# Kernel optimization log

Hardware: AMD Instinct MI355X
Metric: run time of the kernel (lower is better)

Reference implementation:

```python
import math
import jax, jax.numpy as jnp
import numpy as np

V, BS, L, C, H, B, T = 50257, 2048, 4, 768, 12, 2, 2048
D = C // H


def layer_norm(x, g, b, eps=1e-5):
    m = x.mean(-1, keepdims=True)
    v = ((x - m) ** 2).mean(-1, keepdims=True)
    return (x - m) / jnp.sqrt(v + eps) * g + b


def setup_inputs() -> dict:
    key = jax.random.key(0)
    ks = jax.random.split(key, 10)
    s = 0.02
    inp = {}
    inp["idx"] = jax.random.randint(ks[0], (B, T), 0, V)
    inp["tok_emb"] = jax.random.normal(ks[1], (V, C), jnp.float32) * s
    inp["pos_emb"] = jax.random.normal(ks[2], (BS, C), jnp.float32) * s
    inp["ln1_g"] = jnp.ones((L, C)); inp["ln1_b"] = jnp.zeros((L, C))
    inp["qkv_w"] = jax.random.normal(ks[3], (L, C, 3 * C), jnp.float32) * s
    inp["qkv_b"] = jnp.zeros((L, 3 * C))
    inp["aproj_w"] = jax.random.normal(ks[4], (L, C, C), jnp.float32) * s
    inp["aproj_b"] = jnp.zeros((L, C))
    inp["ln2_g"] = jnp.ones((L, C)); inp["ln2_b"] = jnp.zeros((L, C))
    inp["fc_w"] = jax.random.normal(ks[5], (L, C, 4 * C), jnp.float32) * s
    inp["fc_b"] = jnp.zeros((L, 4 * C))
    inp["mproj_w"] = jax.random.normal(ks[6], (L, 4 * C, C), jnp.float32) * s
    inp["mproj_b"] = jnp.zeros((L, C))
    inp["lnf_g"] = jnp.ones((C,)); inp["lnf_b"] = jnp.zeros((C,))
    inp["head_w"] = jax.random.normal(ks[7], (C, V), jnp.float32) * s
    return inp


def reference(idx, tok_emb, pos_emb, ln1_g, ln1_b, qkv_w, qkv_b, aproj_w, aproj_b,
              ln2_g, ln2_b, fc_w, fc_b, mproj_w, mproj_b, lnf_g, lnf_b, head_w):
    b, t = idx.shape
    x = tok_emb[idx] + pos_emb[:t][None]  # [B,T,C]; dropout p=0 -> identity
    mask = jnp.tril(jnp.ones((t, t), bool))  # causal
    neg_inf = jnp.finfo(x.dtype).min
    n_layer = qkv_w.shape[0]
    for l in range(n_layer):
        h = layer_norm(x, ln1_g[l], ln1_b[l])
        qkv = h @ qkv_w[l] + qkv_b[l]  # [B,T,3C]
        q, k, v = jnp.split(qkv, 3, axis=-1)
        q = q.reshape(b, t, H, D).transpose(0, 2, 1, 3)  # [B,H,T,D]
        k = k.reshape(b, t, H, D).transpose(0, 2, 1, 3)
        v = v.reshape(b, t, H, D).transpose(0, 2, 1, 3)
        att = jnp.einsum('bhqd,bhkd->bhqk', q, k) / math.sqrt(D)
        att = jnp.where(mask, att, neg_inf)
        att = jax.nn.softmax(att, axis=-1)
        y = jnp.einsum('bhqk,bhkd->bhqd', att, v)
        y = y.transpose(0, 2, 1, 3).reshape(b, t, C)
        x = x + (y @ aproj_w[l] + aproj_b[l])
        h2 = layer_norm(x, ln2_g[l], ln2_b[l])
        hid = jax.nn.gelu(h2 @ fc_w[l] + fc_b[l], approximate=False)  # exact erf GELU (torch default)
        x = x + (hid @ mproj_w[l] + mproj_b[l])
    x = layer_norm(x, lnf_g, lnf_b)
    logits = x @ head_w  # [B,T,V]
    return logits
```

## Files before the change

kernel.cpp:

```cpp
#include <hip/hip_runtime.h>
#include <cstdint>
#include <cstddef>

#define Tn 2048
#define Bn 2
#define Hn 12
#define Cn 768
#define Ln 4
#define Vn 50257

typedef unsigned short ushort_t;
typedef __attribute__((ext_vector_type(8))) __bf16 bf16x8;
typedef __attribute__((ext_vector_type(8))) unsigned short u16x8;
typedef __attribute__((ext_vector_type(4))) unsigned short u16x4;
typedef __attribute__((ext_vector_type(4))) float f32x4;

static constexpr size_t QKV_ELEMS = (size_t)Bn * Hn * Tn * 64;
static constexpr size_t OFF_QKV = 0;
static constexpr size_t OFF_APROJ = 1769472;
static constexpr size_t OFF_FC = 2359296;
static constexpr size_t OFF_MPROJ = 4718592;

__device__ inline unsigned short f2bf(float f) {
  unsigned int u = __float_as_uint(f);
  unsigned int r = (u + 0x7fffu + ((u >> 16) & 1u)) >> 16;
  return (unsigned short)r;
}

__device__ inline f32x4 zero4() { f32x4 z; z[0]=0.f; z[1]=0.f; z[2]=0.f; z[3]=0.f; return z; }

__device__ inline void gload_lds16(const ushort_t* g, ushort_t* l) {
  __builtin_amdgcn_global_load_lds(
      (const __attribute__((address_space(1))) void*)g,
      (__attribute__((address_space(3))) void*)l, 16, 0, 0);
}

__device__ inline int swz_lin() {
  int nbm = gridDim.x;
  int lin = blockIdx.y * nbm + blockIdx.x;
  int nwg = nbm * gridDim.y;
  int q = nwg >> 3, r = nwg & 7, x = lin & 7, p = lin >> 3;
  return (x < r ? x * (q + 1) : r * (q + 1) + (x - r) * q) + p;
}

__global__ __launch_bounds__(192) void embed_kernel(const int* __restrict__ idx,
    const float* __restrict__ tok, const float* __restrict__ pos, float* __restrict__ x) {
  int row = blockIdx.x;
  int t = row & (Tn - 1);
  int token = idx[row];
  const f32x4* tr = (const f32x4*)(tok + (size_t)token * Cn);
  const f32x4* pr = (const f32x4*)(pos + (size_t)t * Cn);
  f32x4* xr = (f32x4*)(x + (size_t)row * Cn);
  xr[threadIdx.x] = tr[threadIdx.x] + pr[threadIdx.x];
}

__global__ __launch_bounds__(256) void ln_kernel(const float* __restrict__ x,
    const float* __restrict__ gam, const float* __restrict__ bet, ushort_t* __restrict__ out) {
  const int wv = threadIdx.x >> 6, lane = threadIdx.x & 63;
  const int row = blockIdx.x * 4 + wv;
  const f32x4* xr = (const f32x4*)(x + (size_t)row * Cn);
  f32x4 v[3]; float s = 0.f, s2 = 0.f;
  #pragma unroll
  for (int e = 0; e < 3; ++e) {
    v[e] = xr[lane + e*64];
    #pragma unroll
    for (int j = 0; j < 4; ++j) { s += v[e][j]; s2 += v[e][j]*v[e][j]; }
  }
  #pragma unroll
  for (int off = 32; off >= 1; off >>= 1) { s += __shfl_xor(s, off); s2 += __shfl_xor(s2, off); }
  float mean = s * (1.f / Cn);
  float var  = s2 * (1.f / Cn) - mean * mean;
  float rstd = rsqrtf(var + 1e-5f);
  const f32x4* g4 = (const f32x4*)gam;
  const f32x4* b4 = (const f32x4*)bet;
  u16x4* o4 = (u16x4*)(out + (size_t)row * Cn);
  #pragma unroll
  for (int e = 0; e < 3; ++e) {
    f32x4 gv = g4[lane + e*64], bv = b4[lane + e*64];
    u16x4 o;
    #pragma unroll
    for (int j = 0; j < 4; ++j) o[j] = f2bf((v[e][j] - mean) * rstd * gv[j] + bv[j]);
    o4[lane + e*64] = o;
  }
}

__global__ __launch_bounds__(256) void tcvt_kernel(const float* __restrict__ in,
    ushort_t* __restrict__ out, int K, int N, int Npad) {
  __shared__ float tile[32][33];
  int n0 = blockIdx.x * 32, k0 = blockIdx.y * 32;
  int tx = threadIdx.x, ty = threadIdx.y;
  #pragma unroll
  for (int r = 0; r < 4; ++r) {
    int k = k0 + ty + 8*r;
    int n = n0 + tx;
    tile[ty + 8*r][tx] = (n < N) ? in[(size_t)k * N + n] : 0.f;
  }
  __syncthreads();
  #pragma unroll
  for (int r = 0; r < 4; ++r) {
    int n = n0 + ty + 8*r;
    out[(size_t)n * K + k0 + tx] = f2bf(tile[tx][ty + 8*r]);
  }
}

__global__ __launch_bounds__(256) void tcvt4_kernel(const float* __restrict__ qkvp,
    const float* __restrict__ aprojp, const float* __restrict__ fcp,
    const float* __restrict__ mprojp, ushort_t* __restrict__ wT) {
  __shared__ float tile[32][33];
  int bid = blockIdx.x;
  const float* in; int K, N, tilesX, local; size_t ooff;
  if (bid < 1728)      { in = qkvp;   K = 768;  N = 2304; tilesX = 72; ooff = OFF_QKV;   local = bid; }
  else if (bid < 2304) { in = aprojp; K = 768;  N = 768;  tilesX = 24; ooff = OFF_APROJ; local = bid - 1728; }
  else if (bid < 4608) { in = fcp;    K = 768;  N = 3072; tilesX = 96; ooff = OFF_FC;    local = bid - 2304; }
  else                 { in = mprojp; K = 3072; N = 768;  tilesX = 24; ooff = OFF_MPROJ; local = bid - 4608; }
  int n0 = (local % tilesX) * 32, k0 = (local / tilesX) * 32;
  int tx = threadIdx.x, ty = threadIdx.y;
  ushort_t* out = wT + ooff;
  #pragma unroll
  for (int r = 0; r < 4; ++r)
    tile[ty + 8*r][tx] = in[(size_t)(k0 + ty + 8*r) * N + n0 + tx];
  __syncthreads();
  #pragma unroll
  for (int r = 0; r < 4; ++r)
    out[(size_t)(n0 + ty + 8*r) * K + k0 + tx] = f2bf(tile[tx][ty + 8*r]);
}

__global__ __launch_bounds__(256) void vtrans_kernel(const ushort_t* __restrict__ vin,
                                                     ushort_t* __restrict__ vout) {
  __shared__ ushort_t tile[64][65];
  int t0 = blockIdx.x * 64;
  size_t bh = blockIdx.y;
  const ushort_t* src = vin + (bh * Tn + t0) * 64;
  int row = threadIdx.x >> 2, c0 = (threadIdx.x & 3) * 16;
  u16x8 a = *(const u16x8*)&src[(size_t)row * 64 + c0];
  u16x8 b = *(const u16x8*)&src[(size_t)row * 64 + c0 + 8];
  #pragma unroll
  for (int j = 0; j < 8; ++j) { tile[row][c0 + j] = a[j]; tile[row][c0 + 8 + j] = b[j]; }
  __syncthreads();
  int d = threadIdx.x >> 2, tq = (threadIdx.x & 3) * 16;
  u16x8 o0, o1;
  #pragma unroll
  for (int j = 0; j < 8; ++j) { o0[j] = tile[tq + j][d]; o1[j] = tile[tq + 8 + j][d]; }
  ushort_t* dst = vout + (bh * 64 + d) * Tn + t0 + tq;
  *(u16x8*)&dst[0] = o0;
  *(u16x8*)&dst[8] = o1;
}

__global__ __launch_bounds__(512, 2) void gemm256_kernel(
    const ushort_t* __restrict__ A, const ushort_t* __restrict__ Bt,
    const float* __restrict__ bias, float* __restrict__ outp,
    int M, int N, int K) {
  __shared__ ushort_t lds[3 * 16384];
  const int t = threadIdx.x;
  const int w = t >> 6, l = t & 63, lo = l & 15, g = l >> 4;
  const int wm = w >> 2, wn = w & 3;

  int bm, bn;
  {
    int seq = swz_lin();
    int gsz = 8 * gridDim.y;
    int grp = seq / gsz;
    int t2 = seq - grp * gsz;
    bn = t2 >> 3;
    bm = grp * 8 + (t2 & 7);
  }

  const ushort_t* gAb = A  + (size_t)bm * 256 * K;
  const ushort_t* gBb = Bt + (size_t)bn * 256 * K;

  f32x4 acc[8][4];
  #pragma unroll
  for (int i = 0; i < 8; ++i)
    #pragma unroll
    for (int j = 0; j < 4; ++j) acc[i][j] = zero4();

  auto stage = [&](int kt, int buf) {
    const int k0 = kt << 5;
    #pragma unroll
    for (int j = 0; j < 2; ++j) {
      const int q = j * 512 + t;
      const int r = q >> 2;
      const int cc = ((q & 3) ^ ((r >> 1) & 3)) << 3;
      gload_lds16(gAb + (size_t)r * K + k0 + cc,
                  &lds[buf * 16384 + j * 4096 + w * 512]);
      gload_lds16(gBb + (size_t)r * K + k0 + cc,
                  &lds[buf * 16384 + 8192 + j * 4096 + w * 512]);
    }
  };
  const int csw = ((lo >> 1) & 3) << 3;
  auto compute = [&](int buf) {
    const ushort_t* as = &lds[buf * 16384];
    const ushort_t* bs = &lds[buf * 16384 + 8192];
    bf16x8 af[8], bfr[4];
    #pragma unroll
    for (int mi = 0; mi < 8; ++mi)
      af[mi] = *(const bf16x8*)&as[(wm*128 + mi*16 + lo) * 32 + ((g*8) ^ csw)];
    #pragma unroll
    for (int ni = 0; ni < 4; ++ni)
      bfr[ni] = *(const bf16x8*)&bs[(wn*64 + ni*16 + lo) * 32 + ((g*8) ^ csw)];
    __builtin_amdgcn_s_setprio(1);
    #pragma unroll
    for (int mi = 0; mi < 8; ++mi)
      #pragma unroll
      for (int ni = 0; ni < 4; ++ni)
        acc[mi][ni] = __builtin_amdgcn_mfma_f32_16x16x32_bf16(af[mi], bfr[ni], acc[mi][ni], 0, 0, 0);
    __builtin_amdgcn_s_setprio(0);
  };

  const int NK = K >> 5;
  stage(0, 0); stage(1, 1); stage(2, 2);
  asm volatile("s_waitcnt vmcnt(8)" ::: "memory");
  __builtin_amdgcn_s_barrier();

  int buf = 0;
  #pragma unroll 1
  for (int kt = 0; kt < NK; ++kt) {
    compute(buf);
    asm volatile("s_waitcnt lgkmcnt(0)" ::: "memory");
    __builtin_amdgcn_s_barrier();
    if (kt + 3 < NK) {
      stage(kt + 3, buf);
      asm volatile("s_waitcnt vmcnt(8)" ::: "memory");
    } else if (kt + 2 < NK) {
      asm volatile("s_waitcnt vmcnt(4)" ::: "memory");
    } else {
      asm volatile("s_waitcnt vmcnt(0)" ::: "memory");
    }
    __builtin_amdgcn_s_barrier();
    buf = (buf == 2) ? 0 : buf + 1;
  }

  #pragma unroll
  for (int mi = 0; mi < 8; ++mi) {
    #pragma unroll
    for (int ni = 0; ni < 4; ++ni) {
      int colg = bn*256 + wn*64 + ni*16 + lo;
      if (colg < N) {
        float bv = bias ? bias[colg] : 0.f;
        #pragma unroll
        for (int i = 0; i < 4; ++i) {
          int rowg = bm*256 + wm*128 + mi*16 + 4*g + i;
          outp[(size_t)rowg * N + colg] = acc[mi][ni][i] + bv;
        }
      }
    }
  }
}

template<int MODE, int TM>
__global__ __launch_bounds__(256) void gemm_kernel(
    const ushort_t* __restrict__ A, const ushort_t* __restrict__ Bt,
    const float* __restrict__ bias, void* __restrict__ outp,
    const float* __restrict__ res, int M, int N, int K) {
  constexpr int MI = TM / 32;
  constexpr int ASZ = TM * 32;
  constexpr int BUFE = ASZ + 4096;
  constexpr int LPT = TM/64 + 2;
  __shared__ ushort_t lds[3 * BUFE];
  const int t = threadIdx.x;
  int bm, bn;
  {
    int seq = swz_lin();
    const int G = 8;
    int gsz = G * gridDim.y;
    int grp = seq / gsz;
    int t2 = seq - grp * gsz;
    bn = t2 / G;
    bm = grp * G + (t2 - bn * G);
  }
  const int w = t >> 6, l = t & 63, lo = l & 15, g = l >> 4;
  const int wm = w >> 1, wn = w & 1;

  f32x4 acc[MI][4];
  #pragma unroll
  for (int i = 0; i < MI; ++i)
    #pragma unroll
    for (int j = 0; j < 4; ++j) acc[i][j] = zero4();

  const ushort_t* gAb = A  + (size_t)bm * TM * K;
  const ushort_t* gBb = Bt + (size_t)bn * 128 * K;

  auto stage = [&](int kt, int buf) {
    const int k0 = kt << 5;
    #pragma unroll
    for (int j = 0; j < TM/64; ++j) {
      const int q = j * 256 + t;
      const int r = q >> 2;
      const int cc = ((q & 3) ^ ((r >> 1) & 3)) << 3;
      gload_lds16(gAb + (size_t)r * K + k0 + cc, &lds[buf*BUFE + (j*256 + w*64)*8]);
    }
    #pragma unroll
    for (int j = 0; j < 2; ++j) {
      const int q = j * 256 + t;
      const int r = q >> 2;
      const int cc = ((q & 3) ^ ((r >> 1) & 3)) << 3;
      gload_lds16(gBb + (size_t)r * K + k0 + cc, &lds[buf*BUFE + ASZ + (j*256 + w*64)*8]);
    }
  };
  const int csw = ((lo >> 1) & 3) << 3;
  auto compute = [&](int buf) {
    const ushort_t* as = &lds[buf * BUFE];
    const ushort_t* bs = &lds[buf * BUFE + ASZ];
    bf16x8 af[MI], bfr[4];
    #pragma unroll
    for (int mi = 0; mi < MI; ++mi)
      af[mi] = *(const bf16x8*)&as[(wm*(TM/2) + mi*16 + lo) * 32 + ((g*8) ^ csw)];
    #pragma unroll
    for (int ni = 0; ni < 4; ++ni)
      bfr[ni] = *(const bf16x8*)&bs[(wn*64 + ni*16 + lo) * 32 + ((g*8) ^ csw)];
    __builtin_amdgcn_s_setprio(1);
    #pragma unroll
    for (int mi = 0; mi < MI; ++mi)
      #pragma unroll
      for (int ni = 0; ni < 4; ++ni)
        acc[mi][ni] = __builtin_amdgcn_mfma_f32_16x16x32_bf16(af[mi], bfr[ni], acc[mi][ni], 0, 0, 0);
    __builtin_amdgcn_s_setprio(0);
  };

  const int NK = K >> 5;
  stage(0, 0); stage(1, 1); stage(2, 2);
  if constexpr (LPT == 4) asm volatile("s_waitcnt vmcnt(8)" ::: "memory");
  else                    asm volatile("s_waitcnt vmcnt(6)" ::: "memory");
  __builtin_amdgcn_s_barrier();

  int buf = 0;
  #pragma unroll 1
  for (int kt = 0; kt < NK; ++kt) {
    compute(buf);
    asm volatile("s_waitcnt lgkmcnt(0)" ::: "memory");
    __builtin_amdgcn_s_barrier();
    if (kt + 3 < NK) {
      stage(kt + 3, buf);
      if constexpr (LPT == 4) asm volatile("s_waitcnt vmcnt(8)" ::: "memory");
      else                    asm volatile("s_waitcnt vmcnt(6)" ::: "memory");
    } else if (kt + 2 < NK) {
      if constexpr (LPT == 4) asm volatile("s_waitcnt vmcnt(4)" ::: "memory");
      else                    asm volatile("s_waitcnt vmcnt(3)" ::: "memory");
    } else {
      asm volatile("s_waitcnt vmcnt(0)" ::: "memory");
    }
    __builtin_amdgcn_s_barrier();
    buf = (buf == 2) ? 0 : buf + 1;
  }

  #pragma unroll
  for (int mi = 0; mi < MI; ++mi) {
    #pragma unroll
    for (int ni = 0; ni < 4; ++ni) {
      int colg = bn*128 + wn*64 + ni*16 + lo;
      if (colg < N) {
        float bv = bias ? bias[colg] : 0.f;
        #pragma unroll
        for (int i = 0; i < 4; ++i) {
          int rowg = bm*TM + wm*(TM/2) + mi*16 + 4*g + i;
          float vv = acc[mi][ni][i] + bv;
          if (MODE == 1) {
            size_t off = (size_t)rowg * N + colg;
            ((float*)outp)[off] = res[off] + vv;
          } else if (MODE == 2) {
            float ge = 0.5f * vv * (1.f + erff(vv * 0.70710678118f));
            ((ushort_t*)outp)[(size_t)rowg * N + colg] = f2bf(ge);
          } else {
            int which = colg / Cn;
            int rem = colg - which * Cn;
            int h = rem >> 6, d = rem & 63;
            int b = rowg >> 11, tt = rowg & (Tn - 1);
            ushort_t* qb = (ushort_t*)outp;
            size_t bh = (size_t)(b * Hn + h);
            size_t off = (bh * Tn + tt) * 64 + d;
            if (which == 0)      qb[off] = f2bf(vv * 0.125f);
            else if (which == 1) qb[QKV_ELEMS + off] = f2bf(vv);
            else                 qb[3*QKV_ELEMS + off] = f2bf(vv);
          }
        }
      }
    }
  }
}

__global__ __launch_bounds__(64) void attn_kernel(const ushort_t* __restrict__ qkvh,
                                                  ushort_t* __restrict__ y) {
  const int l = threadIdx.x;
  const int lo = l & 15, g = l >> 4;
  int nl = swz_lin();
  const int qt = nl & 127;
  const int bh = nl >> 7;
  const int b = bh / Hn, h = bh % Hn;
  const int q0 = qt * 16;
  const ushort_t* Qp = qkvh + (size_t)bh * Tn * 64;
  const ushort_t* Kp = qkvh + QKV_ELEMS + (size_t)bh * Tn * 64;
  const ushort_t* Vt = qkvh + 2*QKV_ELEMS + (size_t)bh * 64 * Tn;

  bf16x8 qf[2];
  #pragma unroll
  for (int ch = 0; ch < 2; ++ch)
    qf[ch] = *(const bf16x8*)&Qp[(size_t)(q0 + lo) * 64 + ch*32 + g*8];

  f32x4 of[4];
  #pragma unroll
  for (int ch = 0; ch < 4; ++ch) of[ch] = zero4();
  float m = -1e30f, lsum = 0.f;
  const int nkv = q0 + 16;
  const bool ghi = (g >= 2);
  const int lg2 = (g & 1) * 32;

  for (int kv0 = 0; kv0 < nkv; kv0 += 32) {
    bf16x8 vf[4];
    #pragma unroll
    for (int ch = 0; ch < 4; ++ch)
      vf[ch] = *(const bf16x8*)&Vt[(size_t)(ch*16 + lo) * Tn + kv0 + g*8];

    float s8[8];
    #pragma unroll
    for (int sub = 0; sub < 2; ++sub) {
      int kvb = kv0 + 16*sub;
      bf16x8 kf[2];
      #pragma unroll
      for (int ch = 0; ch < 2; ++ch)
        kf[ch] = *(const bf16x8*)&Kp[(size_t)(kvb + lo) * 64 + ch*32 + g*8];
      f32x4 st = zero4();
      st = __builtin_amdgcn_mfma_f32_16x16x32_bf16(kf[0], qf[0], st, 0, 0, 0);
      st = __builtin_amdgcn_mfma_f32_16x16x32_bf16(kf[1], qf[1], st, 0, 0, 0);
      #pragma unroll
      for (int i = 0; i < 4; ++i) {
        int kvi = kvb + 4*g + i;
        s8[sub*4 + i] = (kvi <= q0 + lo) ? st[i] : -1e30f;
      }
    }
    float tmax = s8[0];
    #pragma unroll
    for (int j = 1; j < 8; ++j) tmax = fmaxf(tmax, s8[j]);
    tmax = fmaxf(tmax, __shfl_xor(tmax, 16));
    tmax = fmaxf(tmax, __shfl_xor(tmax, 32));
    if (!__all(tmax <= m)) {
      float newm = fmaxf(m, tmax);
      float resc = __expf(m - newm);
      lsum *= resc;
      m = newm;
      #pragma unroll
      for (int i = 0; i < 4; ++i) {
        float rs = __shfl(resc, 4*g + i);
        of[0][i] *= rs; of[1][i] *= rs; of[2][i] *= rs; of[3][i] *= rs;
      }
    }
    float p8[8]; float psum = 0.f;
    #pragma unroll
    for (int j = 0; j < 8; ++j) { p8[j] = __expf(s8[j] - m); psum += p8[j]; }
    psum += __shfl_xor(psum, 16);
    psum += __shfl_xor(psum, 32);
    lsum += psum;
    unsigned int q4[4];
    #pragma unroll
    for (int c = 0; c < 4; ++c)
      asm("v_cvt_pk_bf16_f32 %0, %1, %2" : "=v"(q4[c]) : "v"(p8[2*c]), "v"(p8[2*c+1]));
    union { unsigned int wv[4]; bf16x8 v; } pu;
    #pragma unroll
    for (int j = 0; j < 4; ++j) {
      int srcLane = lo + lg2 + ((j >> 1) << 4);
      unsigned int lo_w = (unsigned int)__shfl((int)q4[j & 1], srcLane);
      unsigned int hi_w = (unsigned int)__shfl((int)q4[2 + (j & 1)], srcLane);
      pu.wv[j] = ghi ? hi_w : lo_w;
    }
    #pragma unroll
    for (int ch = 0; ch < 4; ++ch)
      of[ch] = __builtin_amdgcn_mfma_f32_16x16x32_bf16(pu.v, vf[ch], of[ch], 0, 0, 0);
  }

  #pragma unroll
  for (int i = 0; i < 4; ++i) {
    float li = 1.f / __shfl(lsum, 4*g + i);
    of[0][i] *= li; of[1][i] *= li; of[2][i] *= li; of[3][i] *= li;
  }
  ushort_t* yb = y + ((size_t)b*Tn + q0) * Cn + h*64;
  #pragma unroll
  for (int ch = 0; ch < 4; ++ch)
    #pragma unroll
    for (int i = 0; i < 4; ++i)
      yb[(size_t)(4*g + i) * Cn + ch*16 + lo] = f2bf(of[ch][i]);
}

extern "C" void kernel_launch(void* const* d_in, const int* in_sizes, int n_in,
                              void* d_out, int out_size, void* d_ws, size_t ws_size,
                              hipStream_t stream) {
  const int*   idx     = (const int*)d_in[0];
  const float* tok_emb = (const float*)d_in[1];
  const float* pos_emb = (const float*)d_in[2];
  const float* ln1_g   = (const float*)d_in[3];
  const float* ln1_b   = (const float*)d_in[4];
  const float* qkv_w   = (const float*)d_in[5];
  const float* qkv_b   = (const float*)d_in[6];
  const float* aproj_w = (const float*)d_in[7];
  const float* aproj_b = (const float*)d_in[8];
  const float* ln2_g   = (const float*)d_in[9];
  const float* ln2_b   = (const float*)d_in[10];
  const float* fc_w    = (const float*)d_in[11];
  const float* fc_b    = (const float*)d_in[12];
  const float* mproj_w = (const float*)d_in[13];
  const float* mproj_b = (const float*)d_in[14];
  const float* lnf_g   = (const float*)d_in[15];
  const float* lnf_b   = (const float*)d_in[16];
  const float* head_w  = (const float*)d_in[17];
  float* out = (float*)d_out;

  char* ws = (char*)d_ws;
  float*    x    = (float*)(ws);
  ushort_t* hA   = (ushort_t*)(ws + 12582912);
  ushort_t* hB   = (ushort_t*)(ws + 18874368);
  ushort_t* qkvh = (ushort_t*)(ws + 44040192);
  ushort_t* wT   = (ushort_t*)(ws + 69206016);

  const int M = Bn * Tn;
  dim3 tb(32, 8);

  embed_kernel<<<M, 192, 0, stream>>>(idx, tok_emb, pos_emb, x);
  for (int l = 0; l < Ln; ++l) {
    ln_kernel<<<M/4, 256, 0, stream>>>(x, ln1_g + l*Cn, ln1_b + l*Cn, hA);
    tcvt4_kernel<<<6912, tb, 0, stream>>>(qkv_w + (size_t)l*Cn*3*Cn, aproj_w + (size_t)l*Cn*Cn,
                                          fc_w + (size_t)l*Cn*4*Cn, mproj_w + (size_t)l*4*Cn*Cn, wT);
    gemm_kernel<3,128><<<dim3(M/128, 2304/128), 256, 0, stream>>>(hA, wT + OFF_QKV, qkv_b + (size_t)l*3*Cn, qkvh, nullptr, M, 2304, 768);
    vtrans_kernel<<<dim3(Tn/64, Bn*Hn), 256, 0, stream>>>(qkvh + 3*QKV_ELEMS, qkvh + 2*QKV_ELEMS);
    attn_kernel<<<dim3(128, Bn*Hn), 64, 0, stream>>>(qkvh, hA);
    gemm_kernel<1,64><<<dim3(M/64, 768/128), 256, 0, stream>>>(hA, wT + OFF_APROJ, aproj_b + (size_t)l*Cn, x, x, M, 768, 768);
    ln_kernel<<<M/4, 256, 0, stream>>>(x, ln2_g + l*Cn, ln2_b + l*Cn, hA);
    gemm_kernel<2,128><<<dim3(M/128, 3072/128), 256, 0, stream>>>(hA, wT + OFF_FC, fc_b + (size_t)l*4*Cn, hB, nullptr, M, 3072, 768);
    gemm_kernel<1,64><<<dim3(M/64, 768/128), 256, 0, stream>>>(hB, wT + OFF_MPROJ, mproj_b + (size_t)l*Cn, x, x, M, 768, 3072);
  }
  ln_kernel<<<M/4, 256, 0, stream>>>(x, lnf_g, lnf_b, hA);
  tcvt_kernel<<<dim3(50432/32, 768/32), tb, 0, stream>>>(head_w, wT, 768, Vn, 50432);
  gemm256_kernel<<<dim3(M/256, 50432/256), 512, 0, stream>>>(hA, wT, nullptr, out, M, Vn, 768);
}
```

Before: 1.691 ms.

## Process two query tiles per attention wave and batch all-layer weight conversion

The attention kernel now handles 32 query rows per wave as two 16-row tiles. Each K and V fragment load is shared by both tiles, which halves K/V traffic per query and doubles the MFMA work issued per load. Query tiles are scheduled in reverse order so the longest causal blocks start first. Separately, the four per-layer weight transpose/convert launches become a single launch before the layer loop, and a plain-store GEMM epilogue mode is added but not used. The costs are higher register pressure in the attention kernel and half as many attention blocks to fill the GPU.

```diff
diff --git a/kernel.cpp b/kernel.cpp
--- a/kernel.cpp
+++ b/kernel.cpp
@@ -20,6 +20,7 @@
 static constexpr size_t OFF_APROJ = 1769472;
 static constexpr size_t OFF_FC = 2359296;
 static constexpr size_t OFF_MPROJ = 4718592;
+static constexpr size_t PACK_SZ = 7077888;
 
 __device__ inline unsigned short f2bf(float f) {
   unsigned int u = __float_as_uint(f);
@@ -103,19 +104,21 @@
   }
 }
 
-__global__ __launch_bounds__(256) void tcvt4_kernel(const float* __restrict__ qkvp,
-    const float* __restrict__ aprojp, const float* __restrict__ fcp,
-    const float* __restrict__ mprojp, ushort_t* __restrict__ wT) {
+__global__ __launch_bounds__(256) void tcvtAll_kernel(const float* __restrict__ qkvw,
+    const float* __restrict__ aprojw, const float* __restrict__ fcw,
+    const float* __restrict__ mprojw, ushort_t* __restrict__ wT) {
   __shared__ float tile[32][33];
   int bid = blockIdx.x;
-  const float* in; int K, N, tilesX, local; size_t ooff;
-  if (bid < 1728)      { in = qkvp;   K = 768;  N = 2304; tilesX = 72; ooff = OFF_QKV;   local = bid; }
-  else if (bid < 2304) { in = aprojp; K = 768;  N = 768;  tilesX = 24; ooff = OFF_APROJ; local = bid - 1728; }
-  else if (bid < 4608) { in = fcp;    K = 768;  N = 3072; tilesX = 96; ooff = OFF_FC;    local = bid - 2304; }
-  else                 { in = mprojp; K = 3072; N = 768;  tilesX = 24; ooff = OFF_MPROJ; local = bid - 4608; }
+  const int layer = bid / 6912;
+  int local = bid - layer * 6912;
+  const float* in; int K, N, tilesX; size_t ooff;
+  if (local < 1728)      { in = qkvw   + (size_t)layer*1769472; K = 768;  N = 2304; tilesX = 72; ooff = OFF_QKV; }
+  else if (local < 2304) { in = aprojw + (size_t)layer*589824;  K = 768;  N = 768;  tilesX = 24; ooff = OFF_APROJ; local -= 1728; }
+  else if (local < 4608) { in = fcw    + (size_t)layer*2359296; K = 768;  N = 3072; tilesX = 96; ooff = OFF_FC;    local -= 2304; }
+  else                   { in = mprojw + (size_t)layer*2359296; K = 3072; N = 768;  tilesX = 24; ooff = OFF_MPROJ; local -= 4608; }
   int n0 = (local % tilesX) * 32, k0 = (local / tilesX) * 32;
   int tx = threadIdx.x, ty = threadIdx.y;
-  ushort_t* out = wT + ooff;
+  ushort_t* out = wT + (size_t)layer * PACK_SZ + ooff;
   #pragma unroll
   for (int r = 0; r < 4; ++r)
     tile[ty + 8*r][tx] = in[(size_t)(k0 + ty + 8*r) * N + n0 + tx];
@@ -354,7 +357,9 @@
         for (int i = 0; i < 4; ++i) {
           int rowg = bm*TM + wm*(TM/2) + mi*16 + 4*g + i;
           float vv = acc[mi][ni][i] + bv;
-          if (MODE == 1) {
+          if (MODE == 0) {
+            ((float*)outp)[(size_t)rowg * N + colg] = vv;
+          } else if (MODE == 1) {
             size_t off = (size_t)rowg * N + colg;
             ((float*)outp)[off] = res[off] + vv;
           } else if (MODE == 2) {
@@ -383,24 +388,26 @@
   const int l = threadIdx.x;
   const int lo = l & 15, g = l >> 4;
   int nl = swz_lin();
-  const int qt = nl & 127;
-  const int bh = nl >> 7;
+  const int qt = 63 - (nl & 63);
+  const int bh = nl >> 6;
   const int b = bh / Hn, h = bh % Hn;
-  const int q0 = qt * 16;
+  const int q0 = qt * 32;
   const ushort_t* Qp = qkvh + (size_t)bh * Tn * 64;
   const ushort_t* Kp = qkvh + QKV_ELEMS + (size_t)bh * Tn * 64;
   const ushort_t* Vt = qkvh + 2*QKV_ELEMS + (size_t)bh * 64 * Tn;
 
-  bf16x8 qf[2];
-  #pragma unroll
-  for (int ch = 0; ch < 2; ++ch)
-    qf[ch] = *(const bf16x8*)&Qp[(size_t)(q0 + lo) * 64 + ch*32 + g*8];
-
-  f32x4 of[4];
-  #pragma unroll
-  for (int ch = 0; ch < 4; ++ch) of[ch] = zero4();
-  float m = -1e30f, lsum = 0.f;
-  const int nkv = q0 + 16;
+  bf16x8 qf0[2], qf1[2];
+  #pragma unroll
+  for (int ch = 0; ch < 2; ++ch) {
+    qf0[ch] = *(const bf16x8*)&Qp[(size_t)(q0 + lo) * 64 + ch*32 + g*8];
+    qf1[ch] = *(const bf16x8*)&Qp[(size_t)(q0 + 16 + lo) * 64 + ch*32 + g*8];
+  }
+
+  f32x4 of0[4], of1[4];
+  #pragma unroll
+  for (int ch = 0; ch < 4; ++ch) { of0[ch] = zero4(); of1[ch] = zero4(); }
+  float m0 = -1e30f, m1 = -1e30f, ls0 = 0.f, ls1 = 0.f;
+  const int nkv = q0 + 32;
   const bool ghi = (g >= 2);
   const int lg2 = (g & 1) * 32;
 
@@ -410,7 +417,7 @@
     for (int ch = 0; ch < 4; ++ch)
       vf[ch] = *(const bf16x8*)&Vt[(size_t)(ch*16 + lo) * Tn + kv0 + g*8];
 
-    float s8[8];
+    float s80[8], s81[8];
     #pragma unroll
     for (int sub = 0; sub < 2; ++sub) {
       int kvb = kv0 + 16*sub;
@@ -418,65 +425,99 @@
       #pragma unroll
       for (int ch = 0; ch < 2; ++ch)
         kf[ch] = *(const bf16x8*)&Kp[(size_t)(kvb + lo) * 64 + ch*32 + g*8];
-      f32x4 st = zero4();
-      st = __builtin_amdgcn_mfma_f32_16x16x32_bf16(kf[0], qf[0], st, 0, 0, 0);
-      st = __builtin_amdgcn_mfma_f32_16x16x32_bf16(kf[1], qf[1], st, 0, 0, 0);
+      f32x4 st0 = zero4(), st1 = zero4();
+      st0 = __builtin_amdgcn_mfma_f32_16x16x32_bf16(kf[0], qf0[0], st0, 0, 0, 0);
+      st0 = __builtin_amdgcn_mfma_f32_16x16x32_bf16(kf[1], qf0[1], st0, 0, 0, 0);
+      st1 = __builtin_amdgcn_mfma_f32_16x16x32_bf16(kf[0], qf1[0], st1, 0, 0, 0);
+      st1 = __builtin_amdgcn_mfma_f32_16x16x32_bf16(kf[1], qf1[1], st1, 0, 0, 0);
       #pragma unroll
       for (int i = 0; i < 4; ++i) {
         int kvi = kvb + 4*g + i;
-        s8[sub*4 + i] = (kvi <= q0 + lo) ? st[i] : -1e30f;
+        s80[sub*4 + i] = (kvi <= q0 + lo)      ? st0[i] : -1e30f;
+        s81[sub*4 + i] = (kvi <= q0 + 16 + lo) ? st1[i] : -1e30f;
       }
     }
-    float tmax = s8[0];
-    #pragma unroll
-    for (int j = 1; j < 8; ++j) tmax = fmaxf(tmax, s8[j]);
-    tmax = fmaxf(tmax, __shfl_xor(tmax, 16));
-    tmax = fmaxf(tmax, __shfl_xor(tmax, 32));
-    if (!__all(tmax <= m)) {
-      float newm = fmaxf(m, tmax);
-      float resc = __expf(m - newm);
-      lsum *= resc;
-      m = newm;
+    {
+      float tmax = s80[0];
       #pragma unroll
-      for (int i = 0; i < 4; ++i) {
-        float rs = __shfl(resc, 4*g + i);
-        of[0][i] *= rs; of[1][i] *= rs; of[2][i] *= rs; of[3][i] *= rs;
+      for (int j = 1; j < 8; ++j) tmax = fmaxf(tmax, s80[j]);
+      tmax = fmaxf(tmax, __shfl_xor(tmax, 16));
+      tmax = fmaxf(tmax, __shfl_xor(tmax, 32));
+      if (!__all(tmax <= m0)) {
+        float newm = fmaxf(m0, tmax);
+        float resc = __expf(m0 - newm);
+        ls0 *= resc; m0 = newm;
+        #pragma unroll
+        for (int i = 0; i < 4; ++i) {
+          float rs = __shfl(resc, 4*g + i);
+          of0[0][i] *= rs; of0[1][i] *= rs; of0[2][i] *= rs; of0[3][i] *= rs;
+        }
       }
     }
-    float p8[8]; float psum = 0.f;
-    #pragma unroll
-    for (int j = 0; j < 8; ++j) { p8[j] = __expf(s8[j] - m); psum += p8[j]; }
-    psum += __shfl_xor(psum, 16);
-    psum += __shfl_xor(psum, 32);
-    lsum += psum;
-    unsigned int q4[4];
-    #pragma unroll
-    for (int c = 0; c < 4; ++c)
-      asm("v_cvt_pk_bf16_f32 %0, %1, %2" : "=v"(q4[c]) : "v"(p8[2*c]), "v"(p8[2*c+1]));
-    union { unsigned int wv[4]; bf16x8 v; } pu;
+    {
+      float tmax = s81[0];
+      #pragma unroll
+      for (int j = 1; j < 8; ++j) tmax = fmaxf(tmax, s81[j]);
+      tmax = fmaxf(tmax, __shfl_xor(tmax, 16));
+      tmax = fmaxf(tmax, __shfl_xor(tmax, 32));
+      if (!__all(tmax <= m1)) {
+        float newm = fmaxf(m1, tmax);
+        float resc = __expf(m1 - newm);
+        ls1 *= resc; m1 = newm;
+        #pragma unroll
+        for (int i = 0; i < 4; ++i) {
+          float rs = __shfl(resc, 4*g + i);
+          of1[0][i] *= rs; of1[1][i] *= rs; of1[2][i] *= rs; of1[3][i] *= rs;
+        }
+      }
+    }
+    float p80[8], p81[8]; float ps0 = 0.f, ps1 = 0.f;
+    #pragma unroll
+    for (int j = 0; j < 8; ++j) {
+      p80[j] = __expf(s80[j] - m0); ps0 += p80[j];
+      p81[j] = __expf(s81[j] - m1); ps1 += p81[j];
+    }
+    ps0 += __shfl_xor(ps0, 16); ps0 += __shfl_xor(ps0, 32); ls0 += ps0;
+    ps1 += __shfl_xor(ps1, 16); ps1 += __shfl_xor(ps1, 32); ls1 += ps1;
+    unsigned int q40[4], q41[4];
+    #pragma unroll
+    for (int c = 0; c < 4; ++c) {
+      asm("v_cvt_pk_bf16_f32 %0, %1, %2" : "=v"(q40[c]) : "v"(p80[2*c]), "v"(p80[2*c+1]));
+      asm("v_cvt_pk_bf16_f32 %0, %1, %2" : "=v"(q41[c]) : "v"(p81[2*c]), "v"(p81[2*c+1]));
+    }
+    union U { unsigned int wv[4]; bf16x8 v; } pu0, pu1;
     #pragma unroll
     for (int j = 0; j < 4; ++j) {
       int srcLane = lo + lg2 + ((j >> 1) << 4);
-      unsigned int lo_w = (unsigned int)__shfl((int)q4[j & 1], srcLane);
-      unsigned int hi_w = (unsigned int)__shfl((int)q4[2 + (j & 1)], srcLane);
-      pu.wv[j] = ghi ? hi_w : lo_w;
-    }
-    #pragma unroll
-    for (int ch = 0; ch < 4; ++ch)
-      of[ch] = __builtin_amdgcn_mfma_f32_16x16x32_bf16(pu.v, vf[ch], of[ch], 0, 0, 0);
+      unsigned int lo_w0 = (unsigned int)__shfl((int)q40[j & 1], srcLane);
+      unsigned int hi_w0 = (unsigned int)__shfl((int)q40[2 + (j & 1)], srcLane);
+      pu0.wv[j] = ghi ? hi_w0 : lo_w0;
+      unsigned int lo_w1 = (unsigned int)__shfl((int)q41[j & 1], srcLane);
+      unsigned int hi_w1 = (unsigned int)__shfl((int)q41[2 + (j & 1)], srcLane);
+      pu1.wv[j] = ghi ? hi_w1 : lo_w1;
+    }
+    #pragma unroll
+    for (int ch = 0; ch < 4; ++ch) {
+      of0[ch] = __builtin_amdgcn_mfma_f32_16x16x32_bf16(pu0.v, vf[ch], of0[ch], 0, 0, 0);
+      of1[ch] = __builtin_amdgcn_mfma_f32_16x16x32_bf16(pu1.v, vf[ch], of1[ch], 0, 0, 0);
+    }
   }
 
   #pragma unroll
   for (int i = 0; i < 4; ++i) {
-    float li = 1.f / __shfl(lsum, 4*g + i);
-    of[0][i] *= li; of[1][i] *= li; of[2][i] *= li; of[3][i] *= li;
+    float li0 = 1.f / __shfl(ls0, 4*g + i);
+    float li1 = 1.f / __shfl(ls1, 4*g + i);
+    of0[0][i] *= li0; of0[1][i] *= li0; of0[2][i] *= li0; of0[3][i] *= li0;
+    of1[0][i] *= li1; of1[1][i] *= li1; of1[2][i] *= li1; of1[3][i] *= li1;
   }
   ushort_t* yb = y + ((size_t)b*Tn + q0) * Cn + h*64;
   #pragma unroll
   for (int ch = 0; ch < 4; ++ch)
     #pragma unroll
-    for (int i = 0; i < 4; ++i)
-      yb[(size_t)(4*g + i) * Cn + ch*16 + lo] = f2bf(of[ch][i]);
+    for (int i = 0; i < 4; ++i) {
+      yb[(size_t)(4*g + i) * Cn + ch*16 + lo] = f2bf(of0[ch][i]);
+      yb[(size_t)(16 + 4*g + i) * Cn + ch*16 + lo] = f2bf(of1[ch][i]);
+    }
 }
 
 extern "C" void kernel_launch(void* const* d_in, const int* in_sizes, int n_in,
@@ -513,17 +554,17 @@
   dim3 tb(32, 8);
 
   embed_kernel<<<M, 192, 0, stream>>>(idx, tok_emb, pos_emb, x);
+  tcvtAll_kernel<<<27648, tb, 0, stream>>>(qkv_w, aproj_w, fc_w, mproj_w, wT);
   for (int l = 0; l < Ln; ++l) {
+    ushort_t* wTl = wT + (size_t)l * PACK_SZ;
     ln_kernel<<<M/4, 256, 0, stream>>>(x, ln1_g + l*Cn, ln1_b + l*Cn, hA);
-    tcvt4_kernel<<<6912, tb, 0, stream>>>(qkv_w + (size_t)l*Cn*3*Cn, aproj_w + (size_t)l*Cn*Cn,
-                                          fc_w + (size_t)l*Cn*4*Cn, mproj_w + (size_t)l*4*Cn*Cn, wT);
-    gemm_kernel<3,128><<<dim3(M/128, 2304/128), 256, 0, stream>>>(hA, wT + OFF_QKV, qkv_b + (size_t)l*3*Cn, qkvh, nullptr, M, 2304, 768);
+    gemm_kernel<3,128><<<dim3(M/128, 2304/128), 256, 0, stream>>>(hA, wTl + OFF_QKV, qkv_b + (size_t)l*3*Cn, qkvh, nullptr, M, 2304, 768);
     vtrans_kernel<<<dim3(Tn/64, Bn*Hn), 256, 0, stream>>>(qkvh + 3*QKV_ELEMS, qkvh + 2*QKV_ELEMS);
-    attn_kernel<<<dim3(128, Bn*Hn), 64, 0, stream>>>(qkvh, hA);
-    gemm_kernel<1,64><<<dim3(M/64, 768/128), 256, 0, stream>>>(hA, wT + OFF_APROJ, aproj_b + (size_t)l*Cn, x, x, M, 768, 768);
+    attn_kernel<<<dim3(64, Bn*Hn), 64, 0, stream>>>(qkvh, hA);
+    gemm_kernel<1,64><<<dim3(M/64, 768/128), 256, 0, stream>>>(hA, wTl + OFF_APROJ, aproj_b + (size_t)l*Cn, x, x, M, 768, 768);
     ln_kernel<<<M/4, 256, 0, stream>>>(x, ln2_g + l*Cn, ln2_b + l*Cn, hA);
-    gemm_kernel<2,128><<<dim3(M/128, 3072/128), 256, 0, stream>>>(hA, wT + OFF_FC, fc_b + (size_t)l*4*Cn, hB, nullptr, M, 3072, 768);
-    gemm_kernel<1,64><<<dim3(M/64, 768/128), 256, 0, stream>>>(hB, wT + OFF_MPROJ, mproj_b + (size_t)l*Cn, x, x, M, 768, 3072);
+    gemm_kernel<2,128><<<dim3(M/128, 3072/128), 256, 0, stream>>>(hA, wTl + OFF_FC, fc_b + (size_t)l*4*Cn, hB, nullptr, M, 3072, 768);
+    gemm_kernel<1,64><<<dim3(M/64, 768/128), 256, 0, stream>>>(hB, wTl + OFF_MPROJ, mproj_b + (size_t)l*Cn, x, x, M, 768, 3072);
   }
   ln_kernel<<<M/4, 256, 0, stream>>>(x, lnf_g, lnf_b, hA);
   tcvt_kernel<<<dim3(50432/32, 768/32), tb, 0, stream>>>(head_w, wT, 768, Vn, 50432);
```

Result: faster. 1.609 ms (-4.9%).
